# Performance work log

Measured on AMD Instinct MI355X. Metric: run time of the kernel, lower is better.

Reference implementation:

```python
import jax, jax.numpy as jnp
from jax import lax
import numpy as np

# Problem dims (see init_kwargs)
B, CIN, H, W = 4, 128, 128, 128
COUT, K, STRIDE, PAD, DIL, GROUPS, OG = 128, 3, 1, 1, 1, 1, 2


def setup_inputs() -> dict:
    key = jax.random.key(0)
    k0, k1, k2 = jax.random.split(key, 3)
    x = jax.random.normal(k0, (B, CIN, H, W), dtype=jnp.float32)
    off_ch = 3 * OG * K * K  # with_mask=True -> scale=3 (dy, dx, mask)
    # Small random offset-conv weights so offsets are non-trivial (zero-init would degenerate to plain conv)
    w_off = jax.random.normal(k1, (off_ch, CIN, K, K), dtype=jnp.float32) * 0.01
    b_off = jnp.zeros((off_ch,), jnp.float32)
    stdv = 1.0 / np.sqrt(CIN * K * K)
    weight = jax.random.uniform(k2, (COUT, CIN // GROUPS, K, K), jnp.float32, -stdv, stdv)
    bias = jnp.zeros((COUT,), jnp.float32)
    return {"x": x, "w_off": w_off, "b_off": b_off, "weight": weight, "bias": bias}


def _deform_conv2d(x, offset, mask, weight, bias):
    # x: [B,C,H,W]; offset: [B,2*OG*K2,Ho,Wo]; mask: [B,OG*K2,Ho,Wo]
    Bn, C, Hn, Wn = x.shape
    O = weight.shape[0]
    K2 = K * K
    Ho = (Hn + 2 * PAD - DIL * (K - 1) - 1) // STRIDE + 1
    Wo = (Wn + 2 * PAD - DIL * (K - 1) - 1) // STRIDE + 1
    # torchvision layout: per offset group, per kernel point, (dy, dx) interleaved
    off = offset.reshape(Bn, OG, K2, 2, Ho, Wo)
    kg = (jnp.arange(K) * DIL).astype(x.dtype)
    kyf = jnp.repeat(kg, K)  # [K2] kernel row offset, k2 = i*K + j
    kxf = jnp.tile(kg, K)    # [K2] kernel col offset
    base_y = (jnp.arange(Ho) * STRIDE - PAD).astype(x.dtype)
    base_x = (jnp.arange(Wo) * STRIDE - PAD).astype(x.dtype)
    # sampling coords: [B,OG,K2,Ho,Wo]
    sy = base_y[None, None, None, :, None] + kyf[None, None, :, None, None] + off[:, :, :, 0]
    sx = base_x[None, None, None, None, :] + kxf[None, None, :, None, None] + off[:, :, :, 1]
    y0f = jnp.floor(sy)
    x0f = jnp.floor(sx)
    ly = sy - y0f  # bilinear fractional weights
    lx = sx - x0f
    y0 = y0f.astype(jnp.int32)
    x0 = x0f.astype(jnp.int32)
    Cg = C // OG
    xg = x.reshape(Bn, OG, Cg, Hn * Wn)

    def gather(iy, ix):
        # zero-padding semantics: out-of-range corners contribute 0
        valid = ((iy >= 0) & (iy < Hn) & (ix >= 0) & (ix < Wn)).astype(x.dtype)
        idx = (jnp.clip(iy, 0, Hn - 1) * Wn + jnp.clip(ix, 0, Wn - 1)).reshape(Bn, OG, 1, -1)
        v = jnp.take_along_axis(xg, idx, axis=3).reshape(Bn, OG, Cg, K2, Ho, Wo)
        return v * valid[:, :, None]

    v00 = gather(y0, x0)
    v01 = gather(y0, x0 + 1)
    v10 = gather(y0 + 1, x0)
    v11 = gather(y0 + 1, x0 + 1)
    wy = ly[:, :, None]  # broadcast over channel dim
    wx = lx[:, :, None]
    val = (v00 * (1 - wy) * (1 - wx) + v01 * (1 - wy) * wx
           + v10 * wy * (1 - wx) + v11 * wy * wx)
    # modulated DCNv2: multiply sampled values by sigmoid mask
    val = val * mask.reshape(Bn, OG, 1, K2, Ho, Wo)
    # im2col GEMM: cols [B,G,(C/G)*K2,Ho*Wo] x weight [G,O/G,(C/G)*K2]
    cols = val.reshape(Bn, GROUPS, (C // GROUPS) * K2, Ho * Wo)
    wg = weight.reshape(GROUPS, O // GROUPS, (C // GROUPS) * K2)
    out = jnp.einsum('gok,bgkn->bgon', wg, cols).reshape(Bn, O, Ho, Wo)
    return out + bias[None, :, None, None]


def reference(x, w_off, b_off, weight, bias):
    off_out = lax.conv_general_dilated(
        x, w_off, (STRIDE, STRIDE), [(PAD, PAD), (PAD, PAD)],
        rhs_dilation=(DIL, DIL), dimension_numbers=('NCHW', 'OIHW', 'NCHW')
    ) + b_off[None, :, None, None]
    oh, ow, m = jnp.split(off_out, 3, axis=1)
    offset = jnp.concatenate([oh, ow], axis=1)
    mask = jax.nn.sigmoid(m)
    return _deform_conv2d(x, offset, mask, weight, bias)
```

## Files before the change

kernel.cpp:

```cpp
#include <hip/hip_runtime.h>
#include <math.h>

#define NB 4
#define NC 128
#define NH 128
#define NW 128
#define NHW (NH*NW)
#define NCOUT 128

#define SY_OFF 0
#define SX_OFF 1179648
#define MK_OFF 2359296
#define WOFF_OFF 3538944
#define WMAIN_OFF 3580416
#define XT_OFF 3663360

typedef short short8 __attribute__((ext_vector_type(8)));
typedef float f32x4 __attribute__((ext_vector_type(4)));

__device__ inline short f2bf(float f) {
    unsigned u = __float_as_uint(f);
    u = (u + 0x7FFFu + ((u >> 16) & 1u)) >> 16;
    return (short)u;
}
__device__ inline unsigned pack2(float lo, float hi) {
    unsigned r;
    asm("v_cvt_pk_bf16_f32 %0, %1, %2" : "=v"(r) : "v"(lo), "v"(hi));
    return r;
}
__device__ inline float bflo(unsigned u) { return __uint_as_float(u << 16); }
__device__ inline float bfhi(unsigned u) { return __uint_as_float(u & 0xffff0000u); }
__device__ inline unsigned pkf16(float a, float b) {
    auto h = __builtin_amdgcn_cvt_pkrtz(a, b);
    unsigned r; __builtin_memcpy(&r, &h, 4); return r;
}
__device__ inline float f16f(unsigned s) {
    unsigned short us = (unsigned short)s;
    __fp16 h; __builtin_memcpy(&h, &us, 2); return (float)h;
}
__device__ inline void gload_lds16(const void* g, void* l) {
    __builtin_amdgcn_global_load_lds(
        (const __attribute__((address_space(1))) unsigned int*)g,
        (__attribute__((address_space(3))) unsigned int*)l, 16, 0, 0);
}

__global__ void wtrans_kernel(const float* __restrict__ w_off,
                              const float* __restrict__ weight,
                              float* __restrict__ ws)
{
    int i = blockIdx.x * 256 + threadIdx.x;
    if (i < 36*2304) {
        int s = i / 2304, rem = i - s*2304;
        int row = rem / 36, c = rem - row*36;
        int chunk = s / 9, k2 = s - 9*chunk;
        float v = (row < 54 && c < 32) ? w_off[(row*NC + chunk*32 + c)*9 + k2] : 0.f;
        ((short*)(ws + WOFF_OFF))[i] = f2bf(v);
    } else if (i < 36*2304 + 36*4608) {
        int j = i - 36*2304;
        int s = j / 4608, rem = j - s*4608;
        int row = rem / 36, c = rem - row*36;
        int chunk = s / 9, k2 = s - 9*chunk;
        float v = (c < 32) ? weight[(row*NC + chunk*32 + c)*9 + k2] : 0.f;
        ((short*)(ws + WMAIN_OFF))[j] = f2bf(v);
    }
}

__global__ __launch_bounds__(256) void xtrans_kernel(
    const float* __restrict__ x, float* __restrict__ ws)
{
    short* xT = (short*)(ws + XT_OFF);
    const int bid = blockIdx.x;
    const int ys = bid & 15, cg = (bid >> 4) & 15, b = bid >> 8;
    const int col = threadIdx.x & 127, rr = threadIdx.x >> 7;
    const float* xb = x + ((long)(b*NC + cg*8))*NHW;
#pragma unroll
    for (int yy = 0; yy < 4; ++yy) {
        const int y = ys*8 + yy*2 + rr;
        const float* p = xb + y*NW + col;
        float v[8];
#pragma unroll
        for (int q = 0; q < 8; ++q) v[q] = p[q*NHW];
        uint4 u = make_uint4(pack2(v[0],v[1]), pack2(v[2],v[3]),
                             pack2(v[4],v[5]), pack2(v[6],v[7]));
        *(uint4*)&xT[(((long)(b*16+cg)*NH + y)*NW + col)*8] = u;
    }
}

__global__ __launch_bounds__(512, 4) void offconv_kernel(
    float* __restrict__ ws, const float* __restrict__ b_off)
{
    __shared__ short wslab[2][2304];
    int bid = blockIdx.x;
    bid = (bid & 7) * 64 + (bid >> 3);
    const int b   = bid >> 7;
    const int ho  = bid & 127;
    const int tid = threadIdx.x;
    const int lane = tid & 63;
    const int wid = tid >> 6;
    const int n = lane & 15, g = lane >> 4;
    const int px = wid*16 + n;
    const short* woff = (const short*)(ws + WOFF_OFF);
    const char*  xTb  = (const char*)((const short*)(ws + XT_OFF) + (long)b*16*NHW*8);

    f32x4 acc[4];
#pragma unroll
    for (int rf = 0; rf < 4; ++rf) acc[rf] = (f32x4){0.f,0.f,0.f,0.f};

    auto DMA = [&](int it, int buf) {
        if (tid < 288) gload_lds16(woff + it*2304 + tid*8, &wslab[buf][tid*8]);
    };
    auto LOADB = [&](int it) -> short8 {
        const int chunk = it/9, k2 = it - 9*chunk;
        const int y = ho + k2/3 - 1, xc = px + (k2%3) - 1;
        short8 bf = (short8){0,0,0,0,0,0,0,0};
        if ((unsigned)y < NH && (unsigned)xc < NW)
            bf = *(const short8*)(xTb + ((long)(chunk*4 + g)*NHW + y*NW + xc)*16);
        return bf;
    };

    DMA(0, 0);
    short8 bcur = LOADB(0);
    __syncthreads();

#pragma unroll 1
    for (int it = 0; it < 36; ++it) {
        const int cur = it & 1, nxt = cur ^ 1;
        short8 bnext;
        if (it < 35) { DMA(it+1, nxt); bnext = LOADB(it+1); }
        __builtin_amdgcn_sched_barrier(0);
#pragma unroll
        for (int rf = 0; rf < 4; ++rf) {
            short8 af = *(const short8*)&wslab[cur][(rf*16 + n)*36 + 8*g];
            acc[rf] = __builtin_amdgcn_mfma_f32_16x16x32_bf16(af, bcur, acc[rf], 0,0,0);
        }
        __syncthreads();
        bcur = bnext;
    }

#pragma unroll
    for (int rf = 0; rf < 4; ++rf) {
#pragma unroll
        for (int r = 0; r < 4; ++r) {
            int cout = 16*rf + 4*g + r;
            if (cout >= 54) continue;
            float v = acc[rf][r] + b_off[cout];
            if (cout < 36) {
                int og = cout / 18, rem = cout - 18*og;
                int k2c = rem >> 1, d = cout & 1;
                float base = d ? (float)(px - 1 + (k2c % 3))
                              : (float)(ho - 1 + (k2c / 3));
                ws[(d ? SX_OFF : SY_OFF) + (((b*2+og)*9 + k2c)*NHW) + ho*NW + px] = v + base;
            } else {
                int cc = cout - 36;
                int og = cc / 9, k2c = cc - 9*og;
                ws[MK_OFF + (((b*2+og)*9 + k2c)*NHW) + ho*NW + px] = 1.f/(1.f+expf(-v));
            }
        }
    }
}

__global__ __launch_bounds__(256, 4) void deform_kernel(
    const float* __restrict__ ws_c, float* __restrict__ ws,
    const float* __restrict__ bias, float* __restrict__ out)
{
    __shared__ short4 pI[18][64];
    __shared__ uint2  pWp[18][64];
    __shared__ short  wslab[2][4608];

    int bid = blockIdx.x;
    bid = (bid & 7) * 128 + (bid >> 3);
    const int b   = bid >> 8;
    const int ho  = (bid >> 1) & 127;
    const int wb  = (bid & 1) * 64;
    const int tid = threadIdx.x;
    const int lane = tid & 63;
    const int wid = tid >> 6;
    const int n = lane & 15, g = lane >> 4;
    const int pxl = 16*wid + n;
    const short* wmn = (const short*)(ws + WMAIN_OFF);
    const char*  xTb = (const char*)((const short*)(ws + XT_OFF) + (long)b*16*NHW*8);

    f32x4 acc[8];
#pragma unroll
    for (int rf = 0; rf < 8; ++rf) acc[rf] = (f32x4){0.f,0.f,0.f,0.f};

    auto DMA = [&](int slabIdx, int buf) {
        const short* src = wmn + slabIdx*4608;
        gload_lds16(src + tid*8, &wslab[buf][tid*8]);
        gload_lds16(src + 2048 + tid*8, &wslab[buf][2048 + tid*8]);
        if (tid < 64) gload_lds16(src + 4096 + tid*8, &wslab[buf][4096 + tid*8]);
    };

#define GLOAD(j, G0, G1, G2, G3) do {                                   \
        const int row_ = ((j)/18)*9 + (j)%9;                            \
        const int chunk_ = (j)/9;                                       \
        const short4 I_ = pI[row_][pxl];                                \
        const char* xp_ = xTb + (long)(chunk_*4 + g)*(NHW*16);          \
        G0 = *(const uint4*)(xp_ + (((int)I_.x) << 4));                 \
        G1 = *(const uint4*)(xp_ + (((int)I_.y) << 4));                 \
        G2 = *(const uint4*)(xp_ + (((int)I_.z) << 4));                 \
        G3 = *(const uint4*)(xp_ + (((int)I_.w) << 4));                 \
    } while (0)

#define FIN(j, G0, G1, G2, G3, Adst) do {                               \
        const int row_ = ((j)/18)*9 + (j)%9;                            \
        const uint2 wp_ = *(const uint2*)&pWp[row_][pxl];               \
        const float W0_ = f16f(wp_.x), W1_ = f16f(wp_.x >> 16);         \
        const float W2_ = f16f(wp_.y), W3_ = f16f(wp_.y >> 16);         \
        uint4 u_; unsigned* up_ = (unsigned*)&u_;                       \
        const unsigned* a_ = (const unsigned*)&G0;                      \
        const unsigned* b_ = (const unsigned*)&G1;                      \
        const unsigned* c_ = (const unsigned*)&G2;                      \
        const unsigned* d_ = (const unsigned*)&G3;                      \
        _Pragma("unroll")                                               \
        for (int e = 0; e < 4; ++e) {                                   \
            float lo = W0_*bflo(a_[e]) + W1_*bflo(b_[e])                \
                     + W2_*bflo(c_[e]) + W3_*bflo(d_[e]);               \
            float hi = W0_*bfhi(a_[e]) + W1_*bfhi(b_[e])                \
                     + W2_*bfhi(c_[e]) + W3_*bfhi(d_[e]);               \
            up_[e] = pack2(lo, hi);                                     \
        }                                                               \
        __builtin_memcpy(&Adst, &u_, 16);                               \
    } while (0)

    DMA(0, 0);

    for (int e = tid; e < 1152; e += 256) {
        const int row = e >> 6, p = e & 63;
        const int og = row / 9, k2 = row - 9*og;
        const int sidx = (((b*2+og)*9 + k2)*NHW) + ho*NW + wb + p;
        const float sy = ws[SY_OFF + sidx];
        const float sx = ws[SX_OFF + sidx];
        const float m  = ws[MK_OFF + sidx];
        const float y0f = floorf(sy), x0f = floorf(sx);
        const float ly = sy - y0f, lx = sx - x0f;
        const int y0 = (int)y0f, x0i = (int)x0f;
        const int y1 = y0 + 1, x1 = x0i + 1;
        const bool vy0 = (unsigned)y0 < NH, vy1 = (unsigned)y1 < NH;
        const bool vx0 = (unsigned)x0i < NW, vx1 = (unsigned)x1 < NW;
        const int cy0 = min(max(y0,0),NH-1), cy1 = min(max(y1,0),NH-1);
        const int cx0 = min(max(x0i,0),NW-1), cx1 = min(max(x1,0),NW-1);
        pI[row][p] = make_short4(
            (short)(cy0*NW + cx0), (short)(cy0*NW + cx1),
            (short)(cy1*NW + cx0), (short)(cy1*NW + cx1));
        const float W0 = (vy0 && vx0) ? (1.f-ly)*(1.f-lx)*m : 0.f;
        const float W1 = (vy0 && vx1) ? (1.f-ly)*lx*m       : 0.f;
        const float W2 = (vy1 && vx0) ? ly*(1.f-lx)*m       : 0.f;
        const float W3 = (vy1 && vx1) ? ly*lx*m             : 0.f;
        pWp[row][p] = make_uint2(pkf16(W0, W1), pkf16(W2, W3));
    }
    __syncthreads();

    uint4 Ga0, Ga1, Ga2, Ga3, Gb0, Gb1, Gb2, Gb3;
    short8 Acur, Anxt;
    GLOAD(0, Ga0, Ga1, Ga2, Ga3);
    FIN(0, Ga0, Ga1, Ga2, Ga3, Acur);
    GLOAD(1, Gb0, Gb1, Gb2, Gb3);

#define BODY(it, Ain, Aout, H0, H1, H2, H3, F0, F1, F2, F3) do {        \
        const int cur_ = (it) & 1, nxt_ = cur_ ^ 1;                     \
        if ((it) < 35) DMA((it)+1, nxt_);                               \
        if ((it) < 34) GLOAD((it)+2, F0, F1, F2, F3);                   \
        __builtin_amdgcn_sched_barrier(0);                              \
        _Pragma("unroll")                                               \
        for (int rf = 0; rf < 8; ++rf) {                                \
            short8 bf = *(const short8*)&wslab[cur_][(16*rf + n)*36 + 8*g]; \
            acc[rf] = __builtin_amdgcn_mfma_f32_16x16x32_bf16(Ain, bf, acc[rf], 0,0,0); \
        }                                                               \
        if ((it) < 35) FIN((it)+1, H0, H1, H2, H3, Aout);               \
        if ((it) < 34) {                                                \
            asm volatile("s_waitcnt vmcnt(4) lgkmcnt(0)" ::: "memory"); \
            __builtin_amdgcn_s_barrier();                               \
            __builtin_amdgcn_sched_barrier(0);                          \
        } else if ((it) == 34) {                                        \
            asm volatile("s_waitcnt vmcnt(0) lgkmcnt(0)" ::: "memory"); \
            __builtin_amdgcn_s_barrier();                               \
            __builtin_amdgcn_sched_barrier(0);                          \
        }                                                               \
    } while (0)

#pragma unroll 1
    for (int t = 0; t < 18; ++t) {
        BODY(2*t,     Acur, Anxt, Gb0, Gb1, Gb2, Gb3, Ga0, Ga1, Ga2, Ga3);
        BODY(2*t + 1, Anxt, Acur, Ga0, Ga1, Ga2, Ga3, Gb0, Gb1, Gb2, Gb3);
    }
#undef BODY
#undef GLOAD
#undef FIN

#pragma unroll
    for (int rf = 0; rf < 8; ++rf) {
        const int cout = 16*rf + n;
        const float bb = bias[cout];
        float4 o = make_float4(acc[rf][0]+bb, acc[rf][1]+bb,
                               acc[rf][2]+bb, acc[rf][3]+bb);
        *(float4*)&out[((b*NCOUT + cout)*NH + ho)*NW + wb + 16*wid + 4*g] = o;
    }
}

extern "C" void kernel_launch(void* const* d_in, const int* in_sizes, int n_in,
                              void* d_out, int out_size, void* d_ws, size_t ws_size,
                              hipStream_t stream)
{
    const float* x      = (const float*)d_in[0];
    const float* w_off  = (const float*)d_in[1];
    const float* b_off  = (const float*)d_in[2];
    const float* weight = (const float*)d_in[3];
    const float* bias   = (const float*)d_in[4];
    float* out = (float*)d_out;
    float* ws  = (float*)d_ws;

    hipLaunchKernelGGL(wtrans_kernel, dim3(972), dim3(256), 0, stream,
                       w_off, weight, ws);
    hipLaunchKernelGGL(xtrans_kernel, dim3(1024), dim3(256), 0, stream,
                       x, ws);
    hipLaunchKernelGGL(offconv_kernel, dim3(NB*NH), dim3(512), 0, stream,
                       ws, b_off);
    hipLaunchKernelGGL(deform_kernel, dim3(NB*NH*2), dim3(256), 0, stream,
                       ws, ws, bias, out);
}
```

Measured before the change: 99.80 us.

## Widen deform blocks to full rows, pack bilinear math, relax offconv barriers

The deform kernel now processes a full 128-pixel output row per 512-thread block instead of half-rows with 256 threads. Each weight slab loaded into LDS is therefore shared across twice as many pixels, and the DMA is spread over more threads. Bilinear interpolation now uses packed v_pk_mul/v_pk_fma f32 instructions on pairs of bf16-expanded values. In the offset conv, __syncthreads is replaced with partial waitcnt plus s_barrier so the next prefetch can stay in flight. Tradeoffs: larger blocks may lower occupancy under the launch bounds, and the handwritten waitcnt is fragile.

```diff
diff --git a/kernel.cpp b/kernel.cpp
--- a/kernel.cpp
+++ b/kernel.cpp
@@ -17,6 +17,7 @@
 
 typedef short short8 __attribute__((ext_vector_type(8)));
 typedef float f32x4 __attribute__((ext_vector_type(4)));
+typedef float f32x2 __attribute__((ext_vector_type(2)));
 
 __device__ inline short f2bf(float f) {
     unsigned u = __float_as_uint(f);
@@ -28,8 +29,6 @@
     asm("v_cvt_pk_bf16_f32 %0, %1, %2" : "=v"(r) : "v"(lo), "v"(hi));
     return r;
 }
-__device__ inline float bflo(unsigned u) { return __uint_as_float(u << 16); }
-__device__ inline float bfhi(unsigned u) { return __uint_as_float(u & 0xffff0000u); }
 __device__ inline unsigned pkf16(float a, float b) {
     auto h = __builtin_amdgcn_cvt_pkrtz(a, b);
     unsigned r; __builtin_memcpy(&r, &h, 4); return r;
@@ -37,6 +36,15 @@
 __device__ inline float f16f(unsigned s) {
     unsigned short us = (unsigned short)s;
     __fp16 h; __builtin_memcpy(&h, &us, 2); return (float)h;
+}
+__device__ inline f32x2 pkmul(f32x2 a, f32x2 b) {
+    f32x2 d; asm("v_pk_mul_f32 %0, %1, %2" : "=v"(d) : "v"(a), "v"(b)); return d;
+}
+__device__ inline f32x2 pkfma(f32x2 a, f32x2 b, f32x2 c) {
+    f32x2 d; asm("v_pk_fma_f32 %0, %1, %2, %3" : "=v"(d) : "v"(a), "v"(b), "v"(c)); return d;
+}
+__device__ inline f32x2 cpair(unsigned u) {
+    f32x2 c; c.x = __uint_as_float(u << 16); c.y = __uint_as_float(u); return c;
 }
 __device__ inline void gload_lds16(const void* g, void* l) {
     __builtin_amdgcn_global_load_lds(
@@ -120,7 +128,9 @@
 
     DMA(0, 0);
     short8 bcur = LOADB(0);
-    __syncthreads();
+    asm volatile("s_waitcnt vmcnt(1) lgkmcnt(0)" ::: "memory");
+    __builtin_amdgcn_s_barrier();
+    __builtin_amdgcn_sched_barrier(0);
 
 #pragma unroll 1
     for (int it = 0; it < 36; ++it) {
@@ -133,7 +143,12 @@
             short8 af = *(const short8*)&wslab[cur][(rf*16 + n)*36 + 8*g];
             acc[rf] = __builtin_amdgcn_mfma_f32_16x16x32_bf16(af, bcur, acc[rf], 0,0,0);
         }
-        __syncthreads();
+        __builtin_amdgcn_sched_barrier(0);
+        if (it < 35) {
+            asm volatile("s_waitcnt vmcnt(1) lgkmcnt(0)" ::: "memory");
+            __builtin_amdgcn_s_barrier();
+            __builtin_amdgcn_sched_barrier(0);
+        }
         bcur = bnext;
     }
 
@@ -159,19 +174,18 @@
     }
 }
 
-__global__ __launch_bounds__(256, 4) void deform_kernel(
-    const float* __restrict__ ws_c, float* __restrict__ ws,
-    const float* __restrict__ bias, float* __restrict__ out)
-{
-    __shared__ short4 pI[18][64];
-    __shared__ uint2  pWp[18][64];
+__global__ __launch_bounds__(512, 4) void deform_kernel(
+    float* __restrict__ ws, const float* __restrict__ bias,
+    float* __restrict__ out)
+{
+    __shared__ short4 pI[18][128];
+    __shared__ uint2  pWp[18][128];
     __shared__ short  wslab[2][4608];
 
     int bid = blockIdx.x;
-    bid = (bid & 7) * 128 + (bid >> 3);
-    const int b   = bid >> 8;
-    const int ho  = (bid >> 1) & 127;
-    const int wb  = (bid & 1) * 64;
+    bid = (bid & 7) * 64 + (bid >> 3);
+    const int b   = bid >> 7;
+    const int ho  = bid & 127;
     const int tid = threadIdx.x;
     const int lane = tid & 63;
     const int wid = tid >> 6;
@@ -187,7 +201,6 @@
     auto DMA = [&](int slabIdx, int buf) {
         const short* src = wmn + slabIdx*4608;
         gload_lds16(src + tid*8, &wslab[buf][tid*8]);
-        gload_lds16(src + 2048 + tid*8, &wslab[buf][2048 + tid*8]);
         if (tid < 64) gload_lds16(src + 4096 + tid*8, &wslab[buf][4096 + tid*8]);
     };
 
@@ -205,8 +218,10 @@
 #define FIN(j, G0, G1, G2, G3, Adst) do {                               \
         const int row_ = ((j)/18)*9 + (j)%9;                            \
         const uint2 wp_ = *(const uint2*)&pWp[row_][pxl];               \
-        const float W0_ = f16f(wp_.x), W1_ = f16f(wp_.x >> 16);         \
-        const float W2_ = f16f(wp_.y), W3_ = f16f(wp_.y >> 16);         \
+        const float w0s = f16f(wp_.x), w1s = f16f(wp_.x >> 16);         \
+        const float w2s = f16f(wp_.y), w3s = f16f(wp_.y >> 16);         \
+        const f32x2 W0_ = {w0s, w0s}, W1_ = {w1s, w1s};                 \
+        const f32x2 W2_ = {w2s, w2s}, W3_ = {w3s, w3s};                 \
         uint4 u_; unsigned* up_ = (unsigned*)&u_;                       \
         const unsigned* a_ = (const unsigned*)&G0;                      \
         const unsigned* b_ = (const unsigned*)&G1;                      \
@@ -214,21 +229,21 @@
         const unsigned* d_ = (const unsigned*)&G3;                      \
         _Pragma("unroll")                                               \
         for (int e = 0; e < 4; ++e) {                                   \
-            float lo = W0_*bflo(a_[e]) + W1_*bflo(b_[e])                \
-                     + W2_*bflo(c_[e]) + W3_*bflo(d_[e]);               \
-            float hi = W0_*bfhi(a_[e]) + W1_*bfhi(b_[e])                \
-                     + W2_*bfhi(c_[e]) + W3_*bfhi(d_[e]);               \
-            up_[e] = pack2(lo, hi);                                     \
+            f32x2 r_ = pkmul(cpair(d_[e]), W3_);                        \
+            r_ = pkfma(cpair(c_[e]), W2_, r_);                          \
+            r_ = pkfma(cpair(b_[e]), W1_, r_);                          \
+            r_ = pkfma(cpair(a_[e]), W0_, r_);                          \
+            up_[e] = pack2(r_.x, r_.y);                                 \
         }                                                               \
         __builtin_memcpy(&Adst, &u_, 16);                               \
     } while (0)
 
     DMA(0, 0);
 
-    for (int e = tid; e < 1152; e += 256) {
-        const int row = e >> 6, p = e & 63;
+    for (int e = tid; e < 2304; e += 512) {
+        const int row = e >> 7, p = e & 127;
         const int og = row / 9, k2 = row - 9*og;
-        const int sidx = (((b*2+og)*9 + k2)*NHW) + ho*NW + wb + p;
+        const int sidx = (((b*2+og)*9 + k2)*NHW) + ho*NW + p;
         const float sy = ws[SY_OFF + sidx];
         const float sx = ws[SX_OFF + sidx];
         const float m  = ws[MK_OFF + sidx];
@@ -294,7 +309,7 @@
         const float bb = bias[cout];
         float4 o = make_float4(acc[rf][0]+bb, acc[rf][1]+bb,
                                acc[rf][2]+bb, acc[rf][3]+bb);
-        *(float4*)&out[((b*NCOUT + cout)*NH + ho)*NW + wb + 16*wid + 4*g] = o;
+        *(float4*)&out[((b*NCOUT + cout)*NH + ho)*NW + 16*wid + 4*g] = o;
     }
 }
 
@@ -316,6 +331,6 @@
                        x, ws);
     hipLaunchKernelGGL(offconv_kernel, dim3(NB*NH), dim3(512), 0, stream,
                        ws, b_off);
-    hipLaunchKernelGGL(deform_kernel, dim3(NB*NH*2), dim3(256), 0, stream,
-                       ws, ws, bias, out);
-}
+    hipLaunchKernelGGL(deform_kernel, dim3(NB*NH), dim3(512), 0, stream,
+                       ws, bias, out);
+}
```

New measurement: 94.94 us. 4.9% less time.
